# Performance work log

Hardware: AMD Instinct MI355X
Metric: run time of the kernel (lower is better)

The kernel has to match this reference:

```python
import jax, jax.numpy as jnp
import numpy as np

N = 50000        # nodes
E = 800000       # edges (avg degree 16)
HIDDEN = 256
HEADS = 8
HEAD_DIM = HIDDEN // HEADS


def _linear_params(key, fan_in, fan_out):
    k1, k2 = jax.random.split(key)
    s = 1.0 / np.sqrt(fan_in)
    W = jax.random.uniform(k1, (fan_in, fan_out), jnp.float32, -s, s)
    b = jax.random.uniform(k2, (fan_out,), jnp.float32, -s, s)
    return W, b


def setup_inputs() -> dict:
    key = jax.random.key(0)
    ks = jax.random.split(key, 7)
    h = jax.random.normal(ks[0], (N, HIDDEN), jnp.float32)
    # sparse adjacency nonzeros: row = destination node, col = source node
    row = jnp.sort(jax.random.randint(ks[1], (E,), 0, N))
    col = jax.random.randint(ks[2], (E,), 0, N)
    Wq, bq = _linear_params(ks[3], HIDDEN, HIDDEN)
    Wk, bk = _linear_params(ks[4], HIDDEN, HIDDEN)
    Wv, bv = _linear_params(ks[5], HIDDEN, HIDDEN)
    Wo, bo = _linear_params(ks[6], HIDDEN, HIDDEN)
    return dict(h=h, row=row, col=col, Wq=Wq, bq=bq, Wk=Wk, bk=bk,
                Wv=Wv, bv=bv, Wo=Wo, bo=bo)


def reference(h, row, col, Wq, bq, Wk, bk, Wv, bv, Wo, bo):
    n = h.shape[0]
    scaling = HEAD_DIM ** (-0.5)
    q = ((h @ Wq + bq).reshape(n, HEADS, HEAD_DIM)) * scaling
    k = (h @ Wk + bk).reshape(n, HEADS, HEAD_DIM)
    v = (h @ Wv + bv).reshape(n, HEADS, HEAD_DIM)

    # bsddmm: per-edge, per-head sampled dot product q[dst] . k[src] -> [E, H]
    s = jnp.einsum('ehd,ehd->eh', q[row], k[col])

    # sparse row-wise softmax over each destination node's incoming edges
    m = jax.ops.segment_max(s, row, num_segments=n)          # [N, H]
    p = jnp.exp(s - m[row])                                   # [E, H]
    denom = jax.ops.segment_sum(p, row, num_segments=n)      # [N, H]
    attn = p / denom[row]                                     # [E, H]

    # bspmm: out[dst] = sum over incoming edges attn * v[src] -> [N, H, D]
    out = jax.ops.segment_sum(attn[:, :, None] * v[col], row, num_segments=n)
    return out.reshape(n, HIDDEN) @ Wo + bo
```

## Files before the change

kernel.cpp:

```cpp
#include <hip/hip_runtime.h>
#include <math.h>


typedef __attribute__((ext_vector_type(8))) short bf16x8;
typedef __attribute__((ext_vector_type(4))) float f32x4;

__device__ __forceinline__ ushort f2bf(float f) {
    uint u = __float_as_uint(f);
    u += 0x7fffu + ((u >> 16) & 1u);
    return (ushort)(u >> 16);
}
__device__ __forceinline__ float bflo(uint u) { return __uint_as_float(u << 16); }
__device__ __forceinline__ float bfhi(uint u) { return __uint_as_float(u & 0xffff0000u); }

#if __has_builtin(__builtin_amdgcn_sdot4)
__device__ __forceinline__ int SDOT4(uint a, uint b, int c) {
    return __builtin_amdgcn_sdot4((int)a, (int)b, c, false);
}
#else
__device__ __forceinline__ int SDOT4(uint a, uint b, int c) {
    #pragma unroll
    for (int i = 0; i < 4; ++i)
        c += ((int)(a << (24 - 8 * i)) >> 24) * ((int)(b << (24 - 8 * i)) >> 24);
    return c;
}
#endif

__device__ __forceinline__ void load_lds16(const void* g, void* l) {
    __builtin_amdgcn_global_load_lds(
        (const __attribute__((address_space(1))) void*)g,
        (__attribute__((address_space(3))) void*)l, 16, 0, 0);
}

__global__ __launch_bounds__(256) void convert_bf16(
    const float* __restrict__ in, ushort* __restrict__ out, size_t nelem)
{
    size_t i = ((size_t)blockIdx.x * 256 + threadIdx.x) * 4;
    if (i >= nelem) return;
    float4 v = *(const float4*)(in + i);
    *(ushort4*)(out + i) = make_ushort4(f2bf(v.x), f2bf(v.y), f2bf(v.z), f2bf(v.w));
}

__global__ __launch_bounds__(256) void prep(
    const float* __restrict__ Wq, const float* __restrict__ Wk,
    const float* __restrict__ Wv, const float* __restrict__ Wo,
    const float* __restrict__ bq, const float* __restrict__ bk,
    const float* __restrict__ bv,
    const int* __restrict__ row, int* __restrict__ row_ptr, int n, int E,
    ushort* __restrict__ Wall, ushort* __restrict__ Wot,
    float* __restrict__ ball)
{
    int m = blockIdx.y;
    if (m == 4) {
        int i = blockIdx.x * 256 + threadIdx.x;
        if (i > n) return;
        int lo = 0, hi = E;
        while (lo < hi) {
            int mid = (lo + hi) >> 1;
            if (row[mid] < i) lo = mid + 1; else hi = mid;
        }
        row_ptr[i] = lo;
        return;
    }
    if (blockIdx.x < 256) {
        int idx = blockIdx.x * 256 + threadIdx.x;
        int k = idx >> 8, nn = idx & 255;
        if (m < 3) {
            const float* W = m == 0 ? Wq : (m == 1 ? Wk : Wv);
            Wall[((size_t)m * 256 + nn) * 256 + k] = f2bf(W[idx]);
        } else {
            Wot[nn * 256 + k] = f2bf(Wo[idx]);
        }
    } else if (m < 3) {
        int i = threadIdx.x;
        ball[m * 256 + i] = (m == 0 ? bq : (m == 1 ? bk : bv))[i];
    }
}

template<int MODE>
__global__ __launch_bounds__(256) void gemm_mfma_lds(
    const ushort* __restrict__ A, const ushort* __restrict__ Wt,
    const float* __restrict__ bias, char* __restrict__ qb8,
    float* __restrict__ qscale, uchar* __restrict__ kv,
    float* __restrict__ kscale, float* __restrict__ vscale,
    float* __restrict__ outf, int n, float scale)
{
    __shared__ ushort SH[2 * 128 * 64];
    ushort* As = SH;
    ushort* Bs = SH + 128 * 64;

    const int nwg = gridDim.x * gridDim.y;
    const int orig = blockIdx.y * gridDim.x + blockIdx.x;
    const int xcd = orig & 7, rnd = orig >> 3;
    const int q8 = nwg >> 3, r8 = nwg & 7;
    const int wgid = (xcd < r8 ? xcd * (q8 + 1) : r8 * (q8 + 1) + (xcd - r8) * q8) + rnd;
    const int tx = wgid % gridDim.x;
    const int ty = wgid / gridDim.x;

    const int tid = threadIdx.x;
    const int lane = tid & 63;
    const int wave = tid >> 6;
    const int col0 = tx * 128;
    const int row0 = ty * 128;
    const int fr = lane & 15;
    const int kg = lane >> 4;
    const int wr = (wave >> 1) * 64;
    const int wc = (wave & 1) * 64;

    f32x4 acc[4][4] = {};

    const int srow = tid >> 3;
    const int sc8 = tid & 7;

    for (int kt = 0; kt < 4; ++kt) {
        #pragma unroll
        for (int it = 0; it < 4; ++it) {
            int r = srow + it * 32;
            int chunk = sc8 ^ (r & 7);
            int ar = row0 + r; ar = ar < n ? ar : n - 1;
            load_lds16((const char*)A + (size_t)ar * 512 + kt * 128 + chunk * 16,
                       (char*)As + (it * 256 + tid) * 16);
            load_lds16((const char*)Wt + (size_t)(col0 + r) * 512 + kt * 128 + chunk * 16,
                       (char*)Bs + (it * 256 + tid) * 16);
        }
        __syncthreads();

        #pragma unroll
        for (int ks = 0; ks < 2; ++ks) {
            bf16x8 a[4], b[4];
            #pragma unroll
            for (int i = 0; i < 4; ++i) {
                int r = wr + i * 16 + fr;
                int chunk = (ks * 4 + kg) ^ (r & 7);
                a[i] = *(const bf16x8*)((const char*)As + r * 128 + chunk * 16);
            }
            #pragma unroll
            for (int j = 0; j < 4; ++j) {
                int c = wc + j * 16 + fr;
                int chunk = (ks * 4 + kg) ^ (c & 7);
                b[j] = *(const bf16x8*)((const char*)Bs + c * 128 + chunk * 16);
            }
            #pragma unroll
            for (int i = 0; i < 4; ++i)
                #pragma unroll
                for (int j = 0; j < 4; ++j)
                    acc[i][j] = __builtin_amdgcn_mfma_f32_16x16x32_bf16(
                        a[i], b[j], acc[i][j], 0, 0, 0);
        }
        __syncthreads();
    }

    if constexpr (MODE == 1) {
        #pragma unroll
        for (int j = 0; j < 4; ++j) {
            int gcol = col0 + wc + j * 16 + fr;
            float bj = bias[gcol];
            #pragma unroll
            for (int i = 0; i < 4; ++i) {
                #pragma unroll
                for (int r = 0; r < 4; ++r) {
                    int grow = row0 + wr + i * 16 + kg * 4 + r;
                    if (grow >= n) continue;
                    outf[(size_t)grow * 256 + gcol] = acc[i][j][r] + bj;
                }
            }
        }
        return;
    }

    char* sb = (char*)SH;
    const float sc = (col0 < 256) ? scale : 1.f;

    #pragma unroll
    for (int j = 0; j < 4; ++j) {
        int cw = wc + j * 16 + fr;
        float bj = bias[col0 + cw];
        #pragma unroll
        for (int i = 0; i < 4; ++i) {
            #pragma unroll
            for (int r2 = 0; r2 < 4; ++r2) {
                int lrow = wr + i * 16 + kg * 4 + r2;
                float val = (acc[i][j][r2] + bj) * sc;
                int u = cw >> 3;
                *(ushort*)(sb + lrow * 256 + ((u ^ (lrow & 7)) << 4) +
                           ((cw & 7) << 1)) = f2bf(val);
            }
        }
    }
    __syncthreads();

    if (col0 >= 256 && col0 < 512) {
        int kseg = col0 - 256;
        int khalf = kseg >> 7;
        #pragma unroll
        for (int pass = 0; pass < 2; ++pass) {
            int t = pass * 256 + tid;
            int lrow = t >> 2, sub = t & 3;
            float vals[32];
            #pragma unroll
            for (int uu = 0; uu < 4; ++uu) {
                int u = sub * 4 + uu;
                uint4 d = *(const uint4*)(sb + lrow * 256 + ((u ^ (lrow & 7)) << 4));
                vals[uu*8+0] = bflo(d.x); vals[uu*8+1] = bfhi(d.x);
                vals[uu*8+2] = bflo(d.y); vals[uu*8+3] = bfhi(d.y);
                vals[uu*8+4] = bflo(d.z); vals[uu*8+5] = bfhi(d.z);
                vals[uu*8+6] = bflo(d.w); vals[uu*8+7] = bfhi(d.w);
            }
            float mx = 0.f;
            #pragma unroll
            for (int i = 0; i < 32; ++i) mx = fmaxf(mx, fabsf(vals[i]));
            mx = fmaxf(mx, __shfl_xor(mx, 1));
            mx = fmaxf(mx, __shfl_xor(mx, 2));
            float inv = mx > 0.f ? 127.f / mx : 0.f;
            float scl = mx > 0.f ? mx * (1.f / 127.f) : 0.f;
            uint pk[8];
            #pragma unroll
            for (int w = 0; w < 8; ++w) {
                uint b0 = (uint)__float2int_rn(vals[w*4+0] * inv) & 0xff;
                uint b1 = (uint)__float2int_rn(vals[w*4+1] * inv) & 0xff;
                uint b2 = (uint)__float2int_rn(vals[w*4+2] * inv) & 0xff;
                uint b3 = (uint)__float2int_rn(vals[w*4+3] * inv) & 0xff;
                pk[w] = b0 | (b1 << 8) | (b2 << 16) | (b3 << 24);
            }
            int grow = row0 + lrow;
            if (grow < n) {
                char* dst = (char*)kv + (size_t)grow * 512 + kseg + sub * 32;
                *(uint4*)dst        = make_uint4(pk[0], pk[1], pk[2], pk[3]);
                *(uint4*)(dst + 16) = make_uint4(pk[4], pk[5], pk[6], pk[7]);
                if (sub == 0) kscale[(size_t)grow * 2 + khalf] = scl;
            }
        }
    } else {
        const bool isq = (col0 < 256);
        int seg = isq ? col0 : (col0 - 512);
        #pragma unroll
        for (int pass = 0; pass < 2; ++pass) {
            int t = pass * 256 + tid;
            int lrow = t >> 2, hh = t & 3;
            float vals[32];
            #pragma unroll
            for (int uu = 0; uu < 4; ++uu) {
                int u = hh * 4 + uu;
                uint4 d = *(const uint4*)(sb + lrow * 256 + ((u ^ (lrow & 7)) << 4));
                vals[uu*8+0] = bflo(d.x); vals[uu*8+1] = bfhi(d.x);
                vals[uu*8+2] = bflo(d.y); vals[uu*8+3] = bfhi(d.y);
                vals[uu*8+4] = bflo(d.z); vals[uu*8+5] = bfhi(d.z);
                vals[uu*8+6] = bflo(d.w); vals[uu*8+7] = bfhi(d.w);
            }
            float mx = 0.f;
            #pragma unroll
            for (int i = 0; i < 32; ++i) mx = fmaxf(mx, fabsf(vals[i]));
            float inv = mx > 0.f ? 127.f / mx : 0.f;
            float scl = mx > 0.f ? mx * (1.f / 127.f) : 0.f;
            uint pk[8];
            #pragma unroll
            for (int w = 0; w < 8; ++w) {
                int b0 = __float2int_rn(vals[w*4+0] * inv);
                int b1 = __float2int_rn(vals[w*4+1] * inv);
                int b2 = __float2int_rn(vals[w*4+2] * inv);
                int b3 = __float2int_rn(vals[w*4+3] * inv);
                if (!isq) { b0 += 128; b1 += 128; b2 += 128; b3 += 128; }
                pk[w] = ((uint)b0 & 0xff) | (((uint)b1 & 0xff) << 8) |
                        (((uint)b2 & 0xff) << 16) | (((uint)b3 & 0xff) << 24);
            }
            int grow = row0 + lrow;
            if (grow < n) {
                char* dst = isq ? (qb8 + (size_t)grow * 256 + seg + hh * 32)
                                : ((char*)kv + (size_t)grow * 512 + 256 + seg + hh * 32);
                *(uint4*)dst        = make_uint4(pk[0], pk[1], pk[2], pk[3]);
                *(uint4*)(dst + 16) = make_uint4(pk[4], pk[5], pk[6], pk[7]);
                float* sdst = isq ? qscale : vscale;
                sdst[(size_t)grow * 8 + (seg >> 5) + hh] = scl;
            }
        }
    }
}

__global__ __launch_bounds__(256) void fused_attn(
    const char* __restrict__ qb8, const float* __restrict__ qscale,
    const uchar* __restrict__ kv, const float* __restrict__ kscale,
    const float* __restrict__ vscale, const int* __restrict__ col,
    const int* __restrict__ row_ptr, ushort* __restrict__ agg, int n)
{
    int node = blockIdx.x * 4 + (threadIdx.x >> 6);
    if (node >= n) return;
    int lane = threadIdx.x & 63;
    int p0 = row_ptr[node], p1 = row_ptr[node + 1];

    const int slot = lane >> 4;
    const int l16 = lane & 15;
    const int aoff = l16 * 32;

    uint4 qi = *(const uint4*)(qb8 + (size_t)node * 256 + l16 * 16);
    float qs = qscale[(size_t)node * 8 + (l16 >> 1)];

    float denom = 0.f;
    float cacc = 0.f;
    float acc[16] = {};

#define ISSUE(IDX, K, V, KS, VS)                                               \
    do {                                                                       \
        int src_ = __shfl(cl, (IDX));                                          \
        const char* b_ = (const char*)kv + (size_t)src_ * 512;                 \
        K = *(const uint4*)(b_ + l16 * 16);                                    \
        V = *(const uint4*)(b_ + 256 + l16 * 16);                              \
        KS = kscale[(size_t)src_ * 2 + (l16 >> 3)];                            \
        VS = vscale[(size_t)src_ * 8 + (l16 >> 1)];                            \
    } while (0)

#define CONSUME(VALID, K, V, KS, VS)                                           \
    do {                                                                       \
        int id_ = SDOT4(qi.x, K.x, 0);                                         \
        id_ = SDOT4(qi.y, K.y, id_);                                           \
        id_ = SDOT4(qi.z, K.z, id_);                                           \
        id_ = SDOT4(qi.w, K.w, id_);                                           \
        int it_ = id_ + __shfl_xor(id_, 1);                                    \
        float s_ = (float)it_ * (qs * (KS));                                   \
        float p_ = (VALID) ? __expf(s_) : 0.f;                                 \
        denom += p_;                                                           \
        float ps_ = p_ * (VS);                                                 \
        cacc += ps_;                                                           \
        uint w_;                                                               \
        w_ = V.x;                                                              \
        acc[0]  = fmaf(ps_, (float)(w_ & 0xff),         acc[0]);               \
        acc[1]  = fmaf(ps_, (float)((w_ >> 8) & 0xff),  acc[1]);               \
        acc[2]  = fmaf(ps_, (float)((w_ >> 16) & 0xff), acc[2]);               \
        acc[3]  = fmaf(ps_, (float)(w_ >> 24),          acc[3]);               \
        w_ = V.y;                                                              \
        acc[4]  = fmaf(ps_, (float)(w_ & 0xff),         acc[4]);               \
        acc[5]  = fmaf(ps_, (float)((w_ >> 8) & 0xff),  acc[5]);               \
        acc[6]  = fmaf(ps_, (float)((w_ >> 16) & 0xff), acc[6]);               \
        acc[7]  = fmaf(ps_, (float)(w_ >> 24),          acc[7]);               \
        w_ = V.z;                                                              \
        acc[8]  = fmaf(ps_, (float)(w_ & 0xff),         acc[8]);               \
        acc[9]  = fmaf(ps_, (float)((w_ >> 8) & 0xff),  acc[9]);               \
        acc[10] = fmaf(ps_, (float)((w_ >> 16) & 0xff), acc[10]);              \
        acc[11] = fmaf(ps_, (float)(w_ >> 24),          acc[11]);              \
        w_ = V.w;                                                              \
        acc[12] = fmaf(ps_, (float)(w_ & 0xff),         acc[12]);              \
        acc[13] = fmaf(ps_, (float)((w_ >> 8) & 0xff),  acc[13]);              \
        acc[14] = fmaf(ps_, (float)((w_ >> 16) & 0xff), acc[14]);              \
        acc[15] = fmaf(ps_, (float)(w_ >> 24),          acc[15]);              \
    } while (0)

    for (int bbase = p0; bbase < p1; bbase += 64) {
        int bd = min(64, p1 - bbase);
        int cl = (lane < bd) ? col[bbase + lane] : 0;
        int nch = (bd + 3) >> 2;

        uint4 kA, vA, kB, vB; float ksA, vsA, ksB, vsB;
        ISSUE(slot, kA, vA, ksA, vsA);
        int c = 0;
        for (;;) {
            if (c + 1 < nch) ISSUE((c + 1) * 4 + slot, kB, vB, ksB, vsB);
            CONSUME(c * 4 + slot < bd, kA, vA, ksA, vsA);
            if (++c >= nch) break;
            if (c + 1 < nch) ISSUE((c + 1) * 4 + slot, kA, vA, ksA, vsA);
            CONSUME(c * 4 + slot < bd, kB, vB, ksB, vsB);
            if (++c >= nch) break;
        }
    }
#undef ISSUE
#undef CONSUME

    #pragma unroll
    for (int i = 0; i < 16; ++i) acc[i] = fmaf(-128.f, cacc, acc[i]);
    #pragma unroll
    for (int i = 0; i < 16; ++i) {
        acc[i] += __shfl_xor(acc[i], 16);
        acc[i] += __shfl_xor(acc[i], 32);
    }
    denom += __shfl_xor(denom, 16);
    denom += __shfl_xor(denom, 32);

    if (slot == 0) {
        float inv = denom > 0.f ? 1.f / denom : 0.f;
        uint o[8];
        #pragma unroll
        for (int i = 0; i < 8; ++i)
            o[i] = (uint)f2bf(acc[2 * i] * inv) |
                   ((uint)f2bf(acc[2 * i + 1] * inv) << 16);
        char* ob = (char*)agg + (size_t)node * 512 + aoff;
        *(uint4*)ob        = make_uint4(o[0], o[1], o[2], o[3]);
        *(uint4*)(ob + 16) = make_uint4(o[4], o[5], o[6], o[7]);
    }
}

extern "C" void kernel_launch(void* const* d_in, const int* in_sizes, int n_in,
                              void* d_out, int out_size, void* d_ws, size_t ws_size,
                              hipStream_t stream)
{
    const float* h  = (const float*)d_in[0];
    const int*   row = (const int*)d_in[1];
    const int*   col = (const int*)d_in[2];
    const float* Wq = (const float*)d_in[3];
    const float* bq = (const float*)d_in[4];
    const float* Wk = (const float*)d_in[5];
    const float* bk = (const float*)d_in[6];
    const float* Wv = (const float*)d_in[7];
    const float* bv = (const float*)d_in[8];
    const float* Wo = (const float*)d_in[9];
    const float* bo = (const float*)d_in[10];
    float* out = (float*)d_out;

    const int n = in_sizes[0] / 256;
    const int E = in_sizes[1];
    const size_t NC = (size_t)n * 256;

    char* base = (char*)d_ws;
    char*   qb8    = base;
    uchar*  kv     = (uchar*)(base + (size_t)n * 256);
    float*  qscale = (float*)(base + (size_t)n * 768);
    float*  vscale = (float*)(base + (size_t)n * 800);
    float*  kscale = (float*)(base + (size_t)n * 832);
    ushort* aggb   = (ushort*)(base + (size_t)n * 840);
    ushort* hb     = (ushort*)(base + (size_t)n * 1352);
    ushort* Wall   = (ushort*)(base + (size_t)n * 1864);
    ushort* Wot    = Wall + 768 * 256;
    float*  ball   = (float*)(Wot + 65536);
    int* row_ptr   = (int*)(ball + 768);

    const float scaling = 0.17677669529663687f;

    dim3 blk(256);
    prep<<<dim3(257, 5), blk, 0, stream>>>(Wq, Wk, Wv, Wo, bq, bk, bv,
                                           row, row_ptr, n, E,
                                           Wall, Wot, ball);
    convert_bf16<<<dim3((int)((NC / 4 + 255) / 256)), blk, 0, stream>>>(h, hb, NC);

    const int mtiles = (n + 127) / 128;
    gemm_mfma_lds<0><<<dim3(6, mtiles), blk, 0, stream>>>(
        hb, Wall, ball, qb8, qscale, kv, kscale, vscale, nullptr, n, scaling);

    fused_attn<<<dim3((n + 3) / 4), blk, 0, stream>>>(
        qb8, qscale, kv, kscale, vscale, col, row_ptr, aggb, n);

    gemm_mfma_lds<1><<<dim3(2, mtiles), blk, 0, stream>>>(
        aggb, Wot, bo, nullptr, nullptr, nullptr, nullptr, nullptr, out, n, 1.f);
}
```

Baseline: 155.6 us.

## Store quantized Q/K/V in head-major planes and split attention per head

The projection GEMM epilogue now writes int8 Q, K and V and their scales into per-head planes indexed by head*n+node, so each (head, node) holds a contiguous 64-byte K/V record. The attention kernel launches eight times as many blocks, one head each: 16 edges per wave step with 4 lanes covering the 32 dims. The goals are more parallelism, fewer registers per thread and narrower gathers. In exchange, the column indices and row pointers are re-read once per head, and each gather is a smaller, more scattered transaction.

```diff
diff --git a/kernel.cpp b/kernel.cpp
--- a/kernel.cpp
+++ b/kernel.cpp
@@ -80,9 +80,9 @@
 template<int MODE>
 __global__ __launch_bounds__(256) void gemm_mfma_lds(
     const ushort* __restrict__ A, const ushort* __restrict__ Wt,
-    const float* __restrict__ bias, char* __restrict__ qb8,
-    float* __restrict__ qscale, uchar* __restrict__ kv,
-    float* __restrict__ kscale, float* __restrict__ vscale,
+    const float* __restrict__ bias, char* __restrict__ q8h,
+    float* __restrict__ qs8, uchar* __restrict__ kvh,
+    float* __restrict__ ks8, float* __restrict__ vs8,
     float* __restrict__ outf, int n, float scale)
 {
     __shared__ ushort SH[2 * 128 * 64];
@@ -189,174 +189,129 @@
     }
     __syncthreads();
 
-    if (col0 >= 256 && col0 < 512) {
-        int kseg = col0 - 256;
-        int khalf = kseg >> 7;
-        #pragma unroll
-        for (int pass = 0; pass < 2; ++pass) {
-            int t = pass * 256 + tid;
-            int lrow = t >> 2, sub = t & 3;
-            float vals[32];
-            #pragma unroll
-            for (int uu = 0; uu < 4; ++uu) {
-                int u = sub * 4 + uu;
-                uint4 d = *(const uint4*)(sb + lrow * 256 + ((u ^ (lrow & 7)) << 4));
-                vals[uu*8+0] = bflo(d.x); vals[uu*8+1] = bfhi(d.x);
-                vals[uu*8+2] = bflo(d.y); vals[uu*8+3] = bfhi(d.y);
-                vals[uu*8+4] = bflo(d.z); vals[uu*8+5] = bfhi(d.z);
-                vals[uu*8+6] = bflo(d.w); vals[uu*8+7] = bfhi(d.w);
-            }
-            float mx = 0.f;
-            #pragma unroll
-            for (int i = 0; i < 32; ++i) mx = fmaxf(mx, fabsf(vals[i]));
+    const bool isq = (col0 < 256);
+    const bool isk = (col0 >= 256 && col0 < 512);
+    const int headBase = (isq ? col0 : (isk ? col0 - 256 : col0 - 512)) >> 5;
+
+    #pragma unroll
+    for (int pass = 0; pass < 2; ++pass) {
+        int t = pass * 256 + tid;
+        int lrow = t >> 2, hh = t & 3;
+        float vals[32];
+        #pragma unroll
+        for (int uu = 0; uu < 4; ++uu) {
+            int u = hh * 4 + uu;
+            uint4 d = *(const uint4*)(sb + lrow * 256 + ((u ^ (lrow & 7)) << 4));
+            vals[uu*8+0] = bflo(d.x); vals[uu*8+1] = bfhi(d.x);
+            vals[uu*8+2] = bflo(d.y); vals[uu*8+3] = bfhi(d.y);
+            vals[uu*8+4] = bflo(d.z); vals[uu*8+5] = bfhi(d.z);
+            vals[uu*8+6] = bflo(d.w); vals[uu*8+7] = bfhi(d.w);
+        }
+        float mx = 0.f;
+        #pragma unroll
+        for (int i = 0; i < 32; ++i) mx = fmaxf(mx, fabsf(vals[i]));
+        if (isk) {
             mx = fmaxf(mx, __shfl_xor(mx, 1));
             mx = fmaxf(mx, __shfl_xor(mx, 2));
-            float inv = mx > 0.f ? 127.f / mx : 0.f;
-            float scl = mx > 0.f ? mx * (1.f / 127.f) : 0.f;
-            uint pk[8];
-            #pragma unroll
-            for (int w = 0; w < 8; ++w) {
-                uint b0 = (uint)__float2int_rn(vals[w*4+0] * inv) & 0xff;
-                uint b1 = (uint)__float2int_rn(vals[w*4+1] * inv) & 0xff;
-                uint b2 = (uint)__float2int_rn(vals[w*4+2] * inv) & 0xff;
-                uint b3 = (uint)__float2int_rn(vals[w*4+3] * inv) & 0xff;
-                pk[w] = b0 | (b1 << 8) | (b2 << 16) | (b3 << 24);
-            }
-            int grow = row0 + lrow;
-            if (grow < n) {
-                char* dst = (char*)kv + (size_t)grow * 512 + kseg + sub * 32;
-                *(uint4*)dst        = make_uint4(pk[0], pk[1], pk[2], pk[3]);
-                *(uint4*)(dst + 16) = make_uint4(pk[4], pk[5], pk[6], pk[7]);
-                if (sub == 0) kscale[(size_t)grow * 2 + khalf] = scl;
-            }
-        }
-    } else {
-        const bool isq = (col0 < 256);
-        int seg = isq ? col0 : (col0 - 512);
-        #pragma unroll
-        for (int pass = 0; pass < 2; ++pass) {
-            int t = pass * 256 + tid;
-            int lrow = t >> 2, hh = t & 3;
-            float vals[32];
-            #pragma unroll
-            for (int uu = 0; uu < 4; ++uu) {
-                int u = hh * 4 + uu;
-                uint4 d = *(const uint4*)(sb + lrow * 256 + ((u ^ (lrow & 7)) << 4));
-                vals[uu*8+0] = bflo(d.x); vals[uu*8+1] = bfhi(d.x);
-                vals[uu*8+2] = bflo(d.y); vals[uu*8+3] = bfhi(d.y);
-                vals[uu*8+4] = bflo(d.z); vals[uu*8+5] = bfhi(d.z);
-                vals[uu*8+6] = bflo(d.w); vals[uu*8+7] = bfhi(d.w);
-            }
-            float mx = 0.f;
-            #pragma unroll
-            for (int i = 0; i < 32; ++i) mx = fmaxf(mx, fabsf(vals[i]));
-            float inv = mx > 0.f ? 127.f / mx : 0.f;
-            float scl = mx > 0.f ? mx * (1.f / 127.f) : 0.f;
-            uint pk[8];
-            #pragma unroll
-            for (int w = 0; w < 8; ++w) {
-                int b0 = __float2int_rn(vals[w*4+0] * inv);
-                int b1 = __float2int_rn(vals[w*4+1] * inv);
-                int b2 = __float2int_rn(vals[w*4+2] * inv);
-                int b3 = __float2int_rn(vals[w*4+3] * inv);
-                if (!isq) { b0 += 128; b1 += 128; b2 += 128; b3 += 128; }
-                pk[w] = ((uint)b0 & 0xff) | (((uint)b1 & 0xff) << 8) |
-                        (((uint)b2 & 0xff) << 16) | (((uint)b3 & 0xff) << 24);
-            }
-            int grow = row0 + lrow;
-            if (grow < n) {
-                char* dst = isq ? (qb8 + (size_t)grow * 256 + seg + hh * 32)
-                                : ((char*)kv + (size_t)grow * 512 + 256 + seg + hh * 32);
-                *(uint4*)dst        = make_uint4(pk[0], pk[1], pk[2], pk[3]);
-                *(uint4*)(dst + 16) = make_uint4(pk[4], pk[5], pk[6], pk[7]);
-                float* sdst = isq ? qscale : vscale;
-                sdst[(size_t)grow * 8 + (seg >> 5) + hh] = scl;
-            }
+        }
+        float inv = mx > 0.f ? 127.f / mx : 0.f;
+        float scl = mx > 0.f ? mx * (1.f / 127.f) : 0.f;
+        uint pk[8];
+        #pragma unroll
+        for (int w = 0; w < 8; ++w) {
+            int b0 = __float2int_rn(vals[w*4+0] * inv);
+            int b1 = __float2int_rn(vals[w*4+1] * inv);
+            int b2 = __float2int_rn(vals[w*4+2] * inv);
+            int b3 = __float2int_rn(vals[w*4+3] * inv);
+            if (!isq && !isk) { b0 += 128; b1 += 128; b2 += 128; b3 += 128; }
+            pk[w] = ((uint)b0 & 0xff) | (((uint)b1 & 0xff) << 8) |
+                    (((uint)b2 & 0xff) << 16) | (((uint)b3 & 0xff) << 24);
+        }
+        int grow = row0 + lrow;
+        if (grow < n) {
+            size_t plane = ((size_t)(headBase + hh)) * n + grow;
+            char* dst;
+            if (isq)      dst = q8h + plane * 32;
+            else if (isk) dst = (char*)kvh + plane * 64;
+            else          dst = (char*)kvh + plane * 64 + 32;
+            *(uint4*)dst        = make_uint4(pk[0], pk[1], pk[2], pk[3]);
+            *(uint4*)(dst + 16) = make_uint4(pk[4], pk[5], pk[6], pk[7]);
+            (isq ? qs8 : (isk ? ks8 : vs8))[plane] = scl;
         }
     }
 }
 
 __global__ __launch_bounds__(256) void fused_attn(
-    const char* __restrict__ qb8, const float* __restrict__ qscale,
-    const uchar* __restrict__ kv, const float* __restrict__ kscale,
-    const float* __restrict__ vscale, const int* __restrict__ col,
+    const char* __restrict__ q8h, const float* __restrict__ qs8,
+    const uchar* __restrict__ kvh, const float* __restrict__ ks8,
+    const float* __restrict__ vs8, const int* __restrict__ col,
     const int* __restrict__ row_ptr, ushort* __restrict__ agg, int n)
 {
-    int node = blockIdx.x * 4 + (threadIdx.x >> 6);
+    const int head = blockIdx.x & 7;
+    const int node = (blockIdx.x >> 3) * 4 + (threadIdx.x >> 6);
     if (node >= n) return;
-    int lane = threadIdx.x & 63;
-    int p0 = row_ptr[node], p1 = row_ptr[node + 1];
-
-    const int slot = lane >> 4;
-    const int l16 = lane & 15;
-    const int aoff = l16 * 32;
-
-    uint4 qi = *(const uint4*)(qb8 + (size_t)node * 256 + l16 * 16);
-    float qs = qscale[(size_t)node * 8 + (l16 >> 1)];
+    const int lane = threadIdx.x & 63;
+    const int p0 = row_ptr[node], p1 = row_ptr[node + 1];
+
+    const int slot = lane >> 2;
+    const int dg = lane & 3;
+
+    const size_t hbase = (size_t)head * n;
+    uint2 qi = *(const uint2*)(q8h + (hbase + node) * 32 + dg * 8);
+    float qs = qs8[hbase + node];
 
     float denom = 0.f;
     float cacc = 0.f;
-    float acc[16] = {};
+    float acc[8] = {};
 
 #define ISSUE(IDX, K, V, KS, VS)                                               \
     do {                                                                       \
         int src_ = __shfl(cl, (IDX));                                          \
-        const char* b_ = (const char*)kv + (size_t)src_ * 512;                 \
-        K = *(const uint4*)(b_ + l16 * 16);                                    \
-        V = *(const uint4*)(b_ + 256 + l16 * 16);                              \
-        KS = kscale[(size_t)src_ * 2 + (l16 >> 3)];                            \
-        VS = vscale[(size_t)src_ * 8 + (l16 >> 1)];                            \
+        const char* b_ = (const char*)kvh + (hbase + src_) * 64;               \
+        K = *(const uint2*)(b_ + dg * 8);                                      \
+        V = *(const uint2*)(b_ + 32 + dg * 8);                                 \
+        KS = ks8[hbase + src_];                                                \
+        VS = vs8[hbase + src_];                                                \
     } while (0)
 
 #define CONSUME(VALID, K, V, KS, VS)                                           \
     do {                                                                       \
         int id_ = SDOT4(qi.x, K.x, 0);                                         \
         id_ = SDOT4(qi.y, K.y, id_);                                           \
-        id_ = SDOT4(qi.z, K.z, id_);                                           \
-        id_ = SDOT4(qi.w, K.w, id_);                                           \
-        int it_ = id_ + __shfl_xor(id_, 1);                                    \
-        float s_ = (float)it_ * (qs * (KS));                                   \
+        int t1_ = id_ + __shfl_xor(id_, 1);                                    \
+        int t2_ = t1_ + __shfl_xor(t1_, 2);                                    \
+        float s_ = (float)t2_ * (qs * (KS));                                   \
         float p_ = (VALID) ? __expf(s_) : 0.f;                                 \
         denom += p_;                                                           \
         float ps_ = p_ * (VS);                                                 \
         cacc += ps_;                                                           \
         uint w_;                                                               \
         w_ = V.x;                                                              \
-        acc[0]  = fmaf(ps_, (float)(w_ & 0xff),         acc[0]);               \
-        acc[1]  = fmaf(ps_, (float)((w_ >> 8) & 0xff),  acc[1]);               \
-        acc[2]  = fmaf(ps_, (float)((w_ >> 16) & 0xff), acc[2]);               \
-        acc[3]  = fmaf(ps_, (float)(w_ >> 24),          acc[3]);               \
+        acc[0] = fmaf(ps_, (float)(w_ & 0xff),         acc[0]);                \
+        acc[1] = fmaf(ps_, (float)((w_ >> 8) & 0xff),  acc[1]);                \
+        acc[2] = fmaf(ps_, (float)((w_ >> 16) & 0xff), acc[2]);                \
+        acc[3] = fmaf(ps_, (float)(w_ >> 24),          acc[3]);                \
         w_ = V.y;                                                              \
-        acc[4]  = fmaf(ps_, (float)(w_ & 0xff),         acc[4]);               \
-        acc[5]  = fmaf(ps_, (float)((w_ >> 8) & 0xff),  acc[5]);               \
-        acc[6]  = fmaf(ps_, (float)((w_ >> 16) & 0xff), acc[6]);               \
-        acc[7]  = fmaf(ps_, (float)(w_ >> 24),          acc[7]);               \
-        w_ = V.z;                                                              \
-        acc[8]  = fmaf(ps_, (float)(w_ & 0xff),         acc[8]);               \
-        acc[9]  = fmaf(ps_, (float)((w_ >> 8) & 0xff),  acc[9]);               \
-        acc[10] = fmaf(ps_, (float)((w_ >> 16) & 0xff), acc[10]);              \
-        acc[11] = fmaf(ps_, (float)(w_ >> 24),          acc[11]);              \
-        w_ = V.w;                                                              \
-        acc[12] = fmaf(ps_, (float)(w_ & 0xff),         acc[12]);              \
-        acc[13] = fmaf(ps_, (float)((w_ >> 8) & 0xff),  acc[13]);              \
-        acc[14] = fmaf(ps_, (float)((w_ >> 16) & 0xff), acc[14]);              \
-        acc[15] = fmaf(ps_, (float)(w_ >> 24),          acc[15]);              \
+        acc[4] = fmaf(ps_, (float)(w_ & 0xff),         acc[4]);                \
+        acc[5] = fmaf(ps_, (float)((w_ >> 8) & 0xff),  acc[5]);                \
+        acc[6] = fmaf(ps_, (float)((w_ >> 16) & 0xff), acc[6]);                \
+        acc[7] = fmaf(ps_, (float)(w_ >> 24),          acc[7]);                \
     } while (0)
 
     for (int bbase = p0; bbase < p1; bbase += 64) {
         int bd = min(64, p1 - bbase);
         int cl = (lane < bd) ? col[bbase + lane] : 0;
-        int nch = (bd + 3) >> 2;
-
-        uint4 kA, vA, kB, vB; float ksA, vsA, ksB, vsB;
+        int nch = (bd + 15) >> 4;
+
+        uint2 kA, vA, kB, vB; float ksA, vsA, ksB, vsB;
         ISSUE(slot, kA, vA, ksA, vsA);
         int c = 0;
         for (;;) {
-            if (c + 1 < nch) ISSUE((c + 1) * 4 + slot, kB, vB, ksB, vsB);
-            CONSUME(c * 4 + slot < bd, kA, vA, ksA, vsA);
+            if (c + 1 < nch) ISSUE((c + 1) * 16 + slot, kB, vB, ksB, vsB);
+            CONSUME(c * 16 + slot < bd, kA, vA, ksA, vsA);
             if (++c >= nch) break;
-            if (c + 1 < nch) ISSUE((c + 1) * 4 + slot, kA, vA, ksA, vsA);
-            CONSUME(c * 4 + slot < bd, kB, vB, ksB, vsB);
+            if (c + 1 < nch) ISSUE((c + 1) * 16 + slot, kA, vA, ksA, vsA);
+            CONSUME(c * 16 + slot < bd, kB, vB, ksB, vsB);
             if (++c >= nch) break;
         }
     }
@@ -364,25 +319,28 @@
 #undef CONSUME
 
     #pragma unroll
-    for (int i = 0; i < 16; ++i) acc[i] = fmaf(-128.f, cacc, acc[i]);
-    #pragma unroll
-    for (int i = 0; i < 16; ++i) {
+    for (int i = 0; i < 8; ++i) acc[i] = fmaf(-128.f, cacc, acc[i]);
+    #pragma unroll
+    for (int i = 0; i < 8; ++i) {
+        acc[i] += __shfl_xor(acc[i], 4);
+        acc[i] += __shfl_xor(acc[i], 8);
         acc[i] += __shfl_xor(acc[i], 16);
         acc[i] += __shfl_xor(acc[i], 32);
     }
+    denom += __shfl_xor(denom, 4);
+    denom += __shfl_xor(denom, 8);
     denom += __shfl_xor(denom, 16);
     denom += __shfl_xor(denom, 32);
 
     if (slot == 0) {
         float inv = denom > 0.f ? 1.f / denom : 0.f;
-        uint o[8];
-        #pragma unroll
-        for (int i = 0; i < 8; ++i)
+        uint o[4];
+        #pragma unroll
+        for (int i = 0; i < 4; ++i)
             o[i] = (uint)f2bf(acc[2 * i] * inv) |
                    ((uint)f2bf(acc[2 * i + 1] * inv) << 16);
-        char* ob = (char*)agg + (size_t)node * 512 + aoff;
-        *(uint4*)ob        = make_uint4(o[0], o[1], o[2], o[3]);
-        *(uint4*)(ob + 16) = make_uint4(o[4], o[5], o[6], o[7]);
+        char* ob = (char*)agg + (size_t)node * 512 + head * 64 + dg * 16;
+        *(uint4*)ob = make_uint4(o[0], o[1], o[2], o[3]);
     }
 }
 
@@ -408,17 +366,17 @@
     const size_t NC = (size_t)n * 256;
 
     char* base = (char*)d_ws;
-    char*   qb8    = base;
-    uchar*  kv     = (uchar*)(base + (size_t)n * 256);
-    float*  qscale = (float*)(base + (size_t)n * 768);
-    float*  vscale = (float*)(base + (size_t)n * 800);
-    float*  kscale = (float*)(base + (size_t)n * 832);
-    ushort* aggb   = (ushort*)(base + (size_t)n * 840);
-    ushort* hb     = (ushort*)(base + (size_t)n * 1352);
-    ushort* Wall   = (ushort*)(base + (size_t)n * 1864);
-    ushort* Wot    = Wall + 768 * 256;
-    float*  ball   = (float*)(Wot + 65536);
-    int* row_ptr   = (int*)(ball + 768);
+    char*   q8h  = base;
+    uchar*  kvh  = (uchar*)(base + (size_t)n * 256);
+    float*  qs8  = (float*)(base + (size_t)n * 768);
+    float*  ks8  = (float*)(base + (size_t)n * 800);
+    float*  vs8  = (float*)(base + (size_t)n * 832);
+    ushort* aggb = (ushort*)(base + (size_t)n * 864);
+    ushort* hb   = (ushort*)(base + (size_t)n * 1376);
+    ushort* Wall = (ushort*)(base + (size_t)n * 1888);
+    ushort* Wot  = Wall + 768 * 256;
+    float*  ball = (float*)(Wot + 65536);
+    int* row_ptr = (int*)(ball + 768);
 
     const float scaling = 0.17677669529663687f;
 
@@ -430,10 +388,10 @@
 
     const int mtiles = (n + 127) / 128;
     gemm_mfma_lds<0><<<dim3(6, mtiles), blk, 0, stream>>>(
-        hb, Wall, ball, qb8, qscale, kv, kscale, vscale, nullptr, n, scaling);
-
-    fused_attn<<<dim3((n + 3) / 4), blk, 0, stream>>>(
-        qb8, qscale, kv, kscale, vscale, col, row_ptr, aggb, n);
+        hb, Wall, ball, q8h, qs8, kvh, ks8, vs8, nullptr, n, scaling);
+
+    fused_attn<<<dim3(((n + 3) / 4) * 8), blk, 0, stream>>>(
+        q8h, qs8, kvh, ks8, vs8, col, row_ptr, aggb, n);
 
     gemm_mfma_lds<1><<<dim3(2, mtiles), blk, 0, stream>>>(
         aggb, Wot, bo, nullptr, nullptr, nullptr, nullptr, nullptr, out, n, 1.f);
```

Result: slower. 257.3 us (+65.3%).
